# Kernel optimization log

Measured on AMD Instinct MI355X. Metric: run time of the kernel, lower is better.

The kernel has to match this reference:

```python
import jax, jax.numpy as jnp
import numpy as np

EMBED_DIM = 1024
HEAD_DIM = 64


def setup_inputs() -> dict:
    key = jax.random.key(0)
    ks = jax.random.split(key, 7)
    s_in = EMBED_DIM ** -0.5  # torch Linear default init scale
    x = jax.random.normal(ks[0], (4, 4096, EMBED_DIM), dtype=jnp.float32)
    Wk = jax.random.uniform(ks[1], (HEAD_DIM, EMBED_DIM), jnp.float32, -s_in, s_in)
    bk = jax.random.uniform(ks[2], (HEAD_DIM,), jnp.float32, -s_in, s_in)
    Wq = jax.random.uniform(ks[3], (HEAD_DIM, EMBED_DIM), jnp.float32, -s_in, s_in)
    bq = jax.random.uniform(ks[4], (HEAD_DIM,), jnp.float32, -s_in, s_in)
    Wv = jax.random.uniform(ks[5], (HEAD_DIM, EMBED_DIM), jnp.float32, -s_in, s_in)
    bv = jax.random.uniform(ks[6], (HEAD_DIM,), jnp.float32, -s_in, s_in)
    return {"x": x, "Wq": Wq, "bq": bq, "Wk": Wk, "bk": bk, "Wv": Wv, "bv": bv}


def reference(x, Wq, bq, Wk, bk, Wv, bv):
    # torch Linear: y = x @ W.T + b
    q = jnp.einsum('btc,dc->btd', x, Wq) + bq  # [B,T,D]
    k = jnp.einsum('btc,dc->btd', x, Wk) + bk
    v = jnp.einsum('btc,dc->btd', x, Wv) + bv
    scale = HEAD_DIM ** -0.5
    # NOTE: original divides by scale (multiplies by sqrt(head_dim)) -- faithful
    scores = jnp.einsum('btd,bsd->bts', q, k) / scale  # [B,T,T]
    attn_weights = jax.nn.softmax(scores, axis=-1)
    return jnp.einsum('bts,bsd->btd', attn_weights, v)
```

## Files before the change

kernel.cpp:

```cpp
#include <hip/hip_runtime.h>

#define BATCH 4
#define SEQ   4096
#define CDIM  1024
#define DDIM  64
#define NROW  (BATCH * SEQ)
#define SP    72
#define SPB   72

typedef _Float16 f16;
typedef _Float16 f16x8 __attribute__((ext_vector_type(8)));
typedef _Float16 f16x4 __attribute__((ext_vector_type(4)));
typedef __fp16   h16x2 __attribute__((ext_vector_type(2)));
typedef float    f32x4 __attribute__((ext_vector_type(4)));

#define MFMA16(a, b, c) __builtin_amdgcn_mfma_f32_16x16x32_f16((a), (b), (c), 0, 0, 0)

#define QSCALE 11.5415603f

__device__ inline f16x8 cvt8(f32x4 a, f32x4 b) {
  h16x2 p0 = __builtin_amdgcn_cvt_pkrtz(a[0], a[1]);
  h16x2 p1 = __builtin_amdgcn_cvt_pkrtz(a[2], a[3]);
  h16x2 p2 = __builtin_amdgcn_cvt_pkrtz(b[0], b[1]);
  h16x2 p3 = __builtin_amdgcn_cvt_pkrtz(b[2], b[3]);
  f16x8 r;
  r[0] = p0[0]; r[1] = p0[1]; r[2] = p1[0]; r[3] = p1[1];
  r[4] = p2[0]; r[5] = p2[1]; r[6] = p3[0]; r[7] = p3[1];
  return r;
}

__device__ inline f16x4 cvt4(float a, float b, float c, float d) {
  h16x2 lo = __builtin_amdgcn_cvt_pkrtz(a, b);
  h16x2 hi = __builtin_amdgcn_cvt_pkrtz(c, d);
  f16x4 r;
  r[0] = lo[0]; r[1] = lo[1]; r[2] = hi[0]; r[3] = hi[1];
  return r;
}

__global__ __launch_bounds__(256) void proj_kernel(const float* __restrict__ x,
                                                   const float* __restrict__ Wq,
                                                   const float* __restrict__ Wk,
                                                   const float* __restrict__ Wv,
                                                   const float* __restrict__ bq,
                                                   const float* __restrict__ bk,
                                                   const float* __restrict__ bv,
                                                   f16* __restrict__ qs,
                                                   f16* __restrict__ ks,
                                                   f16* __restrict__ vT) {
  __shared__ __attribute__((aligned(16))) f16 lw[192][SP];
  const int tid = threadIdx.x;
  const int lane = tid & 63, w = tid >> 6;
  const int n = lane & 15, quad = lane >> 4;
  const int rowbase = blockIdx.x * 64 + w * 16;
  const int srow = tid >> 2;
  const int scol = (tid & 3) * 8;

  const float* Wm[3] = {Wq, Wk, Wv};

  f32x4 acc[3][4];
#pragma unroll
  for (int m_ = 0; m_ < 3; ++m_)
#pragma unroll
    for (int t_ = 0; t_ < 4; ++t_) acc[m_][t_] = (f32x4){0.f, 0.f, 0.f, 0.f};

  const float* xrow = x + (size_t)(rowbase + n) * CDIM + quad * 8;

  f32x4 wr[3][2];
  f32x4 xr0, xr1;
#define WLOAD(KC)                                                          \
  {                                                                        \
    _Pragma("unroll") for (int i = 0; i < 3; ++i) {                        \
      const float* p = Wm[i] + (size_t)srow * CDIM + (KC) + scol;          \
      wr[i][0] = *(const f32x4*)p;                                         \
      wr[i][1] = *(const f32x4*)(p + 4);                                   \
    }                                                                      \
  }
#define XLOAD(KC)                          \
  {                                        \
    xr0 = *(const f32x4*)(xrow + (KC));    \
    xr1 = *(const f32x4*)(xrow + (KC) + 4); \
  }

  WLOAD(0);
  XLOAD(0);
  for (int kc = 0; kc < CDIM; kc += 32) {
#pragma unroll
    for (int i = 0; i < 3; ++i) *(f16x8*)&lw[i * 64 + srow][scol] = cvt8(wr[i][0], wr[i][1]);
    __syncthreads();
    if (kc + 32 < CDIM) WLOAD(kc + 32);
    const f16x8 a = cvt8(xr0, xr1);
    if (kc + 32 < CDIM) XLOAD(kc + 32);
#pragma unroll
    for (int mat = 0; mat < 3; ++mat)
#pragma unroll
      for (int tile = 0; tile < 4; ++tile) {
        const f16x8 bf = *(const f16x8*)&lw[mat * 64 + tile * 16 + n][quad * 8];
        acc[mat][tile] = MFMA16(a, bf, acc[mat][tile]);
      }
    __syncthreads();
  }

  const float* bias_p[3] = {bq, bk, bv};
#pragma unroll
  for (int mat = 0; mat < 3; ++mat)
#pragma unroll
    for (int tile = 0; tile < 4; ++tile) {
      const int d = tile * 16 + n;
      const float bias = bias_p[mat][d];
      const int row0 = rowbase + quad * 4;
      f32x4 a = acc[mat][tile];
      if (mat == 0) {
#pragma unroll
        for (int r = 0; r < 4; ++r)
          qs[(size_t)(row0 + r) * DDIM + d] = (f16)((a[r] + bias) * QSCALE);
      } else if (mat == 1) {
#pragma unroll
        for (int r = 0; r < 4; ++r)
          ks[(size_t)(row0 + r) * DDIM + d] = (f16)(a[r] + bias);
      } else {
        const int bb = row0 >> 12;
        const int t = row0 & (SEQ - 1);
        f16x4 pk = cvt4(a[0] + bias, a[1] + bias, a[2] + bias, a[3] + bias);
        *(f16x4*)(vT + (size_t)(bb * 64 + d) * SEQ + t) = pk;
      }
    }
}

template <int NSPLIT>
__global__ __launch_bounds__(256, 2) void attn_kernel(const f16* __restrict__ qs,
                                                      const f16* __restrict__ ks,
                                                      const f16* __restrict__ vT,
                                                      float* __restrict__ outp,
                                                      float* __restrict__ pm,
                                                      float* __restrict__ pl) {
  __shared__ __attribute__((aligned(16))) f16 pb[4][32][SPB];
  const int tid = threadIdx.x, lane = tid & 63, w = tid >> 6;
  const int n = lane & 15, quad = lane >> 4;
  const int split = blockIdx.x & (NSPLIT - 1);
  const int rowgrp = (blockIdx.x / NSPLIT) * 4 + w;
  const int row0 = rowgrp * 32;
  const int bb = row0 >> 12;
  const int kbase = split * (SEQ / NSPLIT);
  const int NC = SEQ / NSPLIT / 64;

  const f16* kb = ks + (size_t)bb * SEQ * DDIM;
  const f16* vb = vT + (size_t)bb * DDIM * SEQ;

  f16x8 qf[2][2];
#pragma unroll
  for (int g = 0; g < 2; ++g)
#pragma unroll
    for (int h = 0; h < 2; ++h)
      qf[g][h] = *(const f16x8*)(qs + (size_t)(row0 + g * 16 + n) * DDIM + h * 32 + quad * 8);

  f32x4 acc[2][4];
  float m[2] = {-1e30f, -1e30f}, ll[2] = {0.f, 0.f};
#pragma unroll
  for (int g = 0; g < 2; ++g)
#pragma unroll
    for (int t = 0; t < 4; ++t) acc[g][t] = (f32x4){0.f, 0.f, 0.f, 0.f};

  f16x8 kfA[4][2], kfB[4][2], vf[4][2];

  auto kload = [&](f16x8(&DST)[4][2], int kb0) {
#pragma unroll
    for (int st = 0; st < 4; ++st)
#pragma unroll
      for (int h = 0; h < 2; ++h)
        DST[st][h] = *(const f16x8*)(kb + (size_t)(kb0 + st * 16 + n) * DDIM + h * 32 + quad * 8);
  };
  auto vload = [&](int kb0) {
#pragma unroll
    for (int t = 0; t < 4; ++t)
#pragma unroll
      for (int kk = 0; kk < 2; ++kk)
        vf[t][kk] = *(const f16x8*)(vb + (size_t)(t * 16 + n) * SEQ + kb0 + kk * 32 + quad * 8);
  };

  auto chunk = [&](f16x8(&KF)[4][2], f16x8(&KN)[4][2], int c) {
    const int kb0 = kbase + c * 64;
    vload(kb0);
    f32x4 s[2][4];
#pragma unroll
    for (int g = 0; g < 2; ++g)
#pragma unroll
      for (int st = 0; st < 4; ++st) {
        f32x4 z = (f32x4){0.f, 0.f, 0.f, 0.f};
        z = MFMA16(KF[st][0], qf[g][0], z);
        s[g][st] = MFMA16(KF[st][1], qf[g][1], z);
      }
    const int cn = (c + 1 < NC) ? (c + 1) : (NC - 1);
    kload(KN, kbase + cn * 64);

    __builtin_amdgcn_wave_barrier();
#pragma unroll
    for (int g = 0; g < 2; ++g) {
      f32x4 mx;
#pragma unroll
      for (int r = 0; r < 4; ++r)
        mx[r] = fmaxf(fmaxf(s[g][0][r], s[g][1][r]), fmaxf(s[g][2][r], s[g][3][r]));
      float mloc = fmaxf(fmaxf(mx[0], mx[1]), fmaxf(mx[2], mx[3]));
      mloc = fmaxf(mloc, __shfl_xor(mloc, 16));
      mloc = fmaxf(mloc, __shfl_xor(mloc, 32));
      const float mnew = fmaxf(m[g], mloc);
      const float alpha = __builtin_amdgcn_exp2f(m[g] - mnew);
      m[g] = mnew;
      float psum = 0.f;
#pragma unroll
      for (int st = 0; st < 4; ++st) {
        f32x4 p;
#pragma unroll
        for (int r = 0; r < 4; ++r) p[r] = __builtin_amdgcn_exp2f(s[g][st][r] - mnew);
        psum += (p[0] + p[1]) + (p[2] + p[3]);
        *(f16x4*)&pb[w][g * 16 + n][st * 16 + quad * 4] = cvt4(p[0], p[1], p[2], p[3]);
      }
      ll[g] = ll[g] * alpha + psum;
#pragma unroll
      for (int t = 0; t < 4; ++t) acc[g][t] *= alpha;
    }
    __builtin_amdgcn_wave_barrier();
#pragma unroll
    for (int g = 0; g < 2; ++g) {
      const f16x8 pa0 = *(const f16x8*)&pb[w][g * 16 + n][quad * 8];
      const f16x8 pa1 = *(const f16x8*)&pb[w][g * 16 + n][32 + quad * 8];
#pragma unroll
      for (int t = 0; t < 4; ++t) {
        acc[g][t] = MFMA16(vf[t][0], pa0, acc[g][t]);
        acc[g][t] = MFMA16(vf[t][1], pa1, acc[g][t]);
      }
    }
  };

  kload(kfA, kbase);
  for (int c = 0; c < NC; c += 2) {
    chunk(kfA, kfB, c);
    chunk(kfB, kfA, c + 1);
  }

  float lred[2];
#pragma unroll
  for (int g = 0; g < 2; ++g) {
    float l = ll[g];
    l += __shfl_xor(l, 16);
    l += __shfl_xor(l, 32);
    lred[g] = l;
  }

  if (NSPLIT == 1) {
#pragma unroll
    for (int g = 0; g < 2; ++g) {
      const float inv = 1.0f / lred[g];
      const int q = row0 + g * 16 + n;
#pragma unroll
      for (int t = 0; t < 4; ++t) {
        f32x4 o = acc[g][t];
#pragma unroll
        for (int r = 0; r < 4; ++r) o[r] *= inv;
        *(f32x4*)(outp + (size_t)q * DDIM + t * 16 + quad * 4) = o;
      }
    }
  } else {
#pragma unroll
    for (int g = 0; g < 2; ++g) {
      const int q = row0 + g * 16 + n;
#pragma unroll
      for (int t = 0; t < 4; ++t)
        *(f32x4*)(outp + ((size_t)split * NROW + q) * DDIM + t * 16 + quad * 4) = acc[g][t];
      if (quad == 0) {
        pm[split * NROW + q] = m[g];
        pl[split * NROW + q] = lred[g];
      }
    }
  }
}

template <int NSPLIT>
__global__ __launch_bounds__(256) void combine_kernel(const float* __restrict__ pacc,
                                                      const float* __restrict__ pm,
                                                      const float* __restrict__ pl,
                                                      float* __restrict__ out) {
  const int idx = blockIdx.x * 256 + threadIdx.x;
  const int row = idx >> 4;
  const int c = (idx & 15) * 4;
  float mm = pm[row];
#pragma unroll
  for (int s = 1; s < NSPLIT; ++s) mm = fmaxf(mm, pm[s * NROW + row]);
  float L = 0.f;
  f32x4 o = (f32x4){0.f, 0.f, 0.f, 0.f};
#pragma unroll
  for (int s = 0; s < NSPLIT; ++s) {
    const float e = __builtin_amdgcn_exp2f(pm[s * NROW + row] - mm);
    L += pl[s * NROW + row] * e;
    const f32x4 a = *(const f32x4*)(pacc + ((size_t)s * NROW + row) * DDIM + c);
#pragma unroll
    for (int j = 0; j < 4; ++j) o[j] += a[j] * e;
  }
  const float inv = 1.0f / L;
#pragma unroll
  for (int j = 0; j < 4; ++j) o[j] *= inv;
  *(f32x4*)(out + (size_t)row * DDIM + c) = o;
}

extern "C" void kernel_launch(void* const* d_in, const int* in_sizes, int n_in,
                              void* d_out, int out_size, void* d_ws, size_t ws_size,
                              hipStream_t stream) {
  const float* x  = (const float*)d_in[0];
  const float* Wq = (const float*)d_in[1];
  const float* bq = (const float*)d_in[2];
  const float* Wk = (const float*)d_in[3];
  const float* bk = (const float*)d_in[4];
  const float* Wv = (const float*)d_in[5];
  const float* bv = (const float*)d_in[6];
  float* out = (float*)d_out;

  f16* qs = (f16*)d_ws;
  f16* ks = qs + (size_t)NROW * DDIM;
  f16* vT = ks + (size_t)NROW * DDIM;
  char* endf16 = (char*)(vT + (size_t)NROW * DDIM);

  float* pacc = (float*)endf16;
  const size_t base = (size_t)(endf16 - (char*)d_ws);
  const size_t need4 = base + (size_t)4 * NROW * (DDIM + 2) * 4;
  const size_t need2 = base + (size_t)2 * NROW * (DDIM + 2) * 4;

  proj_kernel<<<dim3(256), dim3(256), 0, stream>>>(x, Wq, Wk, Wv, bq, bk, bv, qs, ks, vT);

  if (ws_size >= need4) {
    float* pm = pacc + (size_t)4 * NROW * DDIM;
    float* pl = pm + (size_t)4 * NROW;
    attn_kernel<4><<<dim3(128 * 4), dim3(256), 0, stream>>>(qs, ks, vT, pacc, pm, pl);
    combine_kernel<4><<<dim3(NROW * 16 / 256), dim3(256), 0, stream>>>(pacc, pm, pl, out);
  } else if (ws_size >= need2) {
    float* pm = pacc + (size_t)2 * NROW * DDIM;
    float* pl = pm + (size_t)2 * NROW;
    attn_kernel<2><<<dim3(128 * 2), dim3(256), 0, stream>>>(qs, ks, vT, pacc, pm, pl);
    combine_kernel<2><<<dim3(NROW * 16 / 256), dim3(256), 0, stream>>>(pacc, pm, pl, out);
  } else {
    attn_kernel<1><<<dim3(128), dim3(256), 0, stream>>>(qs, ks, vT, out, nullptr, nullptr);
  }
}
```

Baseline: 190.7 us.

## Share K/V tiles through LDS across waves and raise KV split to eight

Each wave previously loaded its own K and V fragments from global memory. The block now cooperatively stages each 64-key K and V chunk into shared memory, with register prefetch of the next chunk and block-level barriers, so the four waves reuse one copy. Occupancy is raised to four blocks per SIMD, and when the workspace allows, the KV sequence is split eight ways instead of four for more parallelism. The trade-off is two __syncthreads per chunk, a larger combine pass, and an odd LDS padding stride (70) that may cause misaligned 16-byte LDS accesses.

```diff
diff --git a/kernel.cpp b/kernel.cpp
--- a/kernel.cpp
+++ b/kernel.cpp
@@ -6,7 +6,7 @@
 #define DDIM  64
 #define NROW  (BATCH * SEQ)
 #define SP    72
-#define SPB   72
+#define SPA   70
 
 typedef _Float16 f16;
 typedef _Float16 f16x8 __attribute__((ext_vector_type(8)));
@@ -127,18 +127,20 @@
 }
 
 template <int NSPLIT>
-__global__ __launch_bounds__(256, 2) void attn_kernel(const f16* __restrict__ qs,
+__global__ __launch_bounds__(256, 4) void attn_kernel(const f16* __restrict__ qs,
                                                       const f16* __restrict__ ks,
                                                       const f16* __restrict__ vT,
                                                       float* __restrict__ outp,
                                                       float* __restrict__ pm,
                                                       float* __restrict__ pl) {
-  __shared__ __attribute__((aligned(16))) f16 pb[4][32][SPB];
+  __shared__ __attribute__((aligned(16))) f16 lk[64][SPA];
+  __shared__ __attribute__((aligned(16))) f16 lv[64][SPA];
+  __shared__ __attribute__((aligned(16))) f16 pb[4][32][SPA];
   const int tid = threadIdx.x, lane = tid & 63, w = tid >> 6;
   const int n = lane & 15, quad = lane >> 4;
-  const int split = blockIdx.x & (NSPLIT - 1);
-  const int rowgrp = (blockIdx.x / NSPLIT) * 4 + w;
-  const int row0 = rowgrp * 32;
+  const int split = blockIdx.x % NSPLIT;
+  const int rowblk = blockIdx.x / NSPLIT;
+  const int row0 = rowblk * 128 + w * 32;
   const int bb = row0 >> 12;
   const int kbase = split * (SEQ / NSPLIT);
   const int NC = SEQ / NSPLIT / 64;
@@ -146,6 +148,11 @@
   const f16* kb = ks + (size_t)bb * SEQ * DDIM;
   const f16* vb = vT + (size_t)bb * DDIM * SEQ;
 
+  const int srow = tid >> 2;
+  const int scol = (tid & 3) * 16;
+  const f16* kgp = kb + (size_t)(kbase + srow) * DDIM + scol;
+  const f16* vgp = vb + (size_t)srow * SEQ + kbase + scol;
+
   f16x8 qf[2][2];
 #pragma unroll
   for (int g = 0; g < 2; ++g)
@@ -160,39 +167,38 @@
 #pragma unroll
     for (int t = 0; t < 4; ++t) acc[g][t] = (f32x4){0.f, 0.f, 0.f, 0.f};
 
-  f16x8 kfA[4][2], kfB[4][2], vf[4][2];
-
-  auto kload = [&](f16x8(&DST)[4][2], int kb0) {
-#pragma unroll
-    for (int st = 0; st < 4; ++st)
-#pragma unroll
-      for (int h = 0; h < 2; ++h)
-        DST[st][h] = *(const f16x8*)(kb + (size_t)(kb0 + st * 16 + n) * DDIM + h * 32 + quad * 8);
+  f16x8 kr0, kr1, vr0, vr1;
+  auto gload = [&](int c) {
+    const f16* kp = kgp + (size_t)c * 64 * DDIM;
+    kr0 = *(const f16x8*)kp;
+    kr1 = *(const f16x8*)(kp + 8);
+    const f16* vp = vgp + c * 64;
+    vr0 = *(const f16x8*)vp;
+    vr1 = *(const f16x8*)(vp + 8);
   };
-  auto vload = [&](int kb0) {
-#pragma unroll
-    for (int t = 0; t < 4; ++t)
-#pragma unroll
-      for (int kk = 0; kk < 2; ++kk)
-        vf[t][kk] = *(const f16x8*)(vb + (size_t)(t * 16 + n) * SEQ + kb0 + kk * 32 + quad * 8);
-  };
-
-  auto chunk = [&](f16x8(&KF)[4][2], f16x8(&KN)[4][2], int c) {
-    const int kb0 = kbase + c * 64;
-    vload(kb0);
+
+  gload(0);
+  for (int c = 0; c < NC; ++c) {
+    *(f16x8*)&lk[srow][scol] = kr0;
+    *(f16x8*)&lk[srow][scol + 8] = kr1;
+    *(f16x8*)&lv[srow][scol] = vr0;
+    *(f16x8*)&lv[srow][scol + 8] = vr1;
+    __syncthreads();
+    if (c + 1 < NC) gload(c + 1);
+
     f32x4 s[2][4];
 #pragma unroll
-    for (int g = 0; g < 2; ++g)
-#pragma unroll
-      for (int st = 0; st < 4; ++st) {
+    for (int st = 0; st < 4; ++st) {
+      const f16x8 klo = *(const f16x8*)&lk[st * 16 + n][quad * 8];
+      const f16x8 khi = *(const f16x8*)&lk[st * 16 + n][32 + quad * 8];
+#pragma unroll
+      for (int g = 0; g < 2; ++g) {
         f32x4 z = (f32x4){0.f, 0.f, 0.f, 0.f};
-        z = MFMA16(KF[st][0], qf[g][0], z);
-        s[g][st] = MFMA16(KF[st][1], qf[g][1], z);
-      }
-    const int cn = (c + 1 < NC) ? (c + 1) : (NC - 1);
-    kload(KN, kbase + cn * 64);
-
-    __builtin_amdgcn_wave_barrier();
+        z = MFMA16(klo, qf[g][0], z);
+        s[g][st] = MFMA16(khi, qf[g][1], z);
+      }
+    }
+
 #pragma unroll
     for (int g = 0; g < 2; ++g) {
       f32x4 mx;
@@ -219,22 +225,20 @@
       for (int t = 0; t < 4; ++t) acc[g][t] *= alpha;
     }
     __builtin_amdgcn_wave_barrier();
+
 #pragma unroll
     for (int g = 0; g < 2; ++g) {
       const f16x8 pa0 = *(const f16x8*)&pb[w][g * 16 + n][quad * 8];
       const f16x8 pa1 = *(const f16x8*)&pb[w][g * 16 + n][32 + quad * 8];
 #pragma unroll
       for (int t = 0; t < 4; ++t) {
-        acc[g][t] = MFMA16(vf[t][0], pa0, acc[g][t]);
-        acc[g][t] = MFMA16(vf[t][1], pa1, acc[g][t]);
-      }
-    }
-  };
-
-  kload(kfA, kbase);
-  for (int c = 0; c < NC; c += 2) {
-    chunk(kfA, kfB, c);
-    chunk(kfB, kfA, c + 1);
+        const f16x8 vlo = *(const f16x8*)&lv[t * 16 + n][quad * 8];
+        const f16x8 vhi = *(const f16x8*)&lv[t * 16 + n][32 + quad * 8];
+        acc[g][t] = MFMA16(vlo, pa0, acc[g][t]);
+        acc[g][t] = MFMA16(vhi, pa1, acc[g][t]);
+      }
+    }
+    __syncthreads();
   }
 
   float lred[2];
@@ -320,21 +324,21 @@
 
   float* pacc = (float*)endf16;
   const size_t base = (size_t)(endf16 - (char*)d_ws);
+  const size_t need8 = base + (size_t)8 * NROW * (DDIM + 2) * 4;
   const size_t need4 = base + (size_t)4 * NROW * (DDIM + 2) * 4;
-  const size_t need2 = base + (size_t)2 * NROW * (DDIM + 2) * 4;
 
   proj_kernel<<<dim3(256), dim3(256), 0, stream>>>(x, Wq, Wk, Wv, bq, bk, bv, qs, ks, vT);
 
-  if (ws_size >= need4) {
+  if (ws_size >= need8) {
+    float* pm = pacc + (size_t)8 * NROW * DDIM;
+    float* pl = pm + (size_t)8 * NROW;
+    attn_kernel<8><<<dim3(128 * 8), dim3(256), 0, stream>>>(qs, ks, vT, pacc, pm, pl);
+    combine_kernel<8><<<dim3(NROW * 16 / 256), dim3(256), 0, stream>>>(pacc, pm, pl, out);
+  } else if (ws_size >= need4) {
     float* pm = pacc + (size_t)4 * NROW * DDIM;
     float* pl = pm + (size_t)4 * NROW;
     attn_kernel<4><<<dim3(128 * 4), dim3(256), 0, stream>>>(qs, ks, vT, pacc, pm, pl);
     combine_kernel<4><<<dim3(NROW * 16 / 256), dim3(256), 0, stream>>>(pacc, pm, pl, out);
-  } else if (ws_size >= need2) {
-    float* pm = pacc + (size_t)2 * NROW * DDIM;
-    float* pl = pm + (size_t)2 * NROW;
-    attn_kernel<2><<<dim3(128 * 2), dim3(256), 0, stream>>>(qs, ks, vT, pacc, pm, pl);
-    combine_kernel<2><<<dim3(NROW * 16 / 256), dim3(256), 0, stream>>>(pacc, pm, pl, out);
   } else {
     attn_kernel<1><<<dim3(128), dim3(256), 0, stream>>>(qs, ks, vT, out, nullptr, nullptr);
   }
```

Result: faster. 168.8 us (-11.5%).
